# Kernel optimization log

Measured on AMD Instinct MI355X. Metric: run time of the kernel, lower is better.

## Reference

```python
import jax, jax.numpy as jnp
import numpy as np

C = 128   # channels
C4 = C // 4

def setup_inputs() -> dict:
    key = jax.random.key(0)
    k1, k2, k3, k4, k5 = jax.random.split(key, 5)
    B, N = 16, 2048
    x_h = jax.random.normal(k1, (B, C, N), dtype=jnp.float32)
    x_o = jax.random.normal(k2, (B, C, N), dtype=jnp.float32)
    # q_conv and k_conv share the SAME weight (tied in __init__), bias=False
    w_qk = jax.random.normal(k3, (C4, C), dtype=jnp.float32) * (1.0 / np.sqrt(C))
    # v_conv: Conv1d(C, C, 1) with bias
    w_v = jax.random.normal(k4, (C, C), dtype=jnp.float32) * (1.0 / np.sqrt(C))
    b_v = jax.random.normal(k5, (C,), dtype=jnp.float32) * 0.01
    return {"x_h": x_h, "x_o": x_o, "w_qk": w_qk, "w_v": w_v, "b_v": b_v}

def reference(x_h, x_o, w_qk, w_v, b_v):
    # SA_Layer_1 forward (only layer used by Grasp_Transformer_Last.forward)
    # 1x1 conv == channel matmul
    xh_q = jnp.einsum('dc,bcn->bnd', w_qk, x_h)            # [B, Nh, C4]
    xo_k = jnp.einsum('dc,bcm->bdm', w_qk, x_o)            # [B, C4, No]
    alpha = jnp.einsum('bnd,bdm->bnm', xh_q, xo_k)         # [B, Nh, No]
    # no softmax: normalize by column sums over dim=1 (Nh axis)
    attention = alpha / (1e-9 + jnp.sum(alpha, axis=1, keepdims=True))
    xo_v = jnp.einsum('dc,bcm->bmd', w_v, x_o) + b_v       # [B, No, C]
    x_r = jnp.einsum('bnm,bmd->bnd', attention, xo_v)      # [B, Nh, C]
    x_r = jnp.transpose(x_r, (0, 2, 1))                    # [B, C, Nh]
    return (x_r, attention)
```

## Files before the change

### kernel.cpp

```cpp
#include <hip/hip_runtime.h>

constexpr int NTOK = 2048;
constexpr int CH   = 128;
constexpr int C4   = 32;
constexpr int NB   = 16;

typedef __attribute__((ext_vector_type(8))) __bf16 bf16x8;
typedef __attribute__((ext_vector_type(4))) float  f32x4;

__device__ __forceinline__ unsigned short f2bf(float f) {
  union { float f; unsigned u; } v; v.f = f;
  unsigned r = v.u + 0x7fffu + ((v.u >> 16) & 1u);
  return (unsigned short)(r >> 16);
}
__device__ __forceinline__ float bf2f(unsigned short h) {
  union { unsigned u; float f; } v; v.u = ((unsigned)h) << 16;
  return v.f;
}

__global__ __launch_bounds__(256) void rs_kernel(const float* __restrict__ x_h,
                                                 double* __restrict__ rowsumH) {
  const int t = threadIdx.x;
  const int c0 = blockIdx.x * 16;
  const int b = blockIdx.y;
  __shared__ double red[4];
  for (int cl = 0; cl < 16; ++cl) {
    const float* rp = x_h + (size_t)(b * CH + c0 + cl) * NTOK;
    double s = 0.0;
    for (int i = 0; i < 2; ++i) {
      float4 v = *(const float4*)(rp + (t + 256 * i) * 4);
      s += (double)v.x + (double)v.y + (double)v.z + (double)v.w;
    }
    for (int off = 1; off <= 32; off <<= 1) s += __shfl_xor(s, off);
    if ((t & 63) == 0) red[t >> 6] = s;
    __syncthreads();
    if (t == 0) rowsumH[b * CH + c0 + cl] = red[0] + red[1] + red[2] + red[3];
    __syncthreads();
  }
}

__global__ __launch_bounds__(256) void p_kernel(const double* __restrict__ rowsumH,
                                                const float* __restrict__ w_qk,
                                                double* __restrict__ P) {
  const int t = threadIdx.x, b = blockIdx.x;
  __shared__ double Sl[C4];
  if (t < C4) {
    double s = 0.0;
    for (int c = 0; c < CH; ++c) s += (double)w_qk[t * CH + c] * rowsumH[b * CH + c];
    Sl[t] = s;
  }
  __syncthreads();
  if (t < CH) {
    double p = 0.0;
    for (int d = 0; d < C4; ++d) p += Sl[d] * (double)w_qk[d * CH + t];
    P[b * CH + t] = p;
  }
}

__global__ __launch_bounds__(256) void prep_qk(const float* __restrict__ x_h,
                                               const float* __restrict__ x_o,
                                               const float* __restrict__ w_qk,
                                               float* __restrict__ xhq_f32,
                                               float* __restrict__ xokT_f32,
                                               unsigned short* __restrict__ xhq_hi,
                                               unsigned short* __restrict__ xokT_hi,
                                               unsigned short* __restrict__ xhq_lo,
                                               unsigned short* __restrict__ xokT_lo) {
  const int t = threadIdx.x;
  const int n0 = blockIdx.x * 64;
  const int b = blockIdx.y;
  const int which = blockIdx.z;
  const float* src = which ? x_o : x_h;
  float* dstf = which ? xokT_f32 : xhq_f32;
  unsigned short* dsth = which ? xokT_hi : xhq_hi;
  unsigned short* dstl = which ? xokT_lo : xhq_lo;

  __shared__ float Xt[CH][64];
  __shared__ float Wl[C4][132];

  for (int i = 0; i < 8; ++i) {
    int flat = t + 256 * i;
    int c = flat >> 4, f4 = flat & 15;
    float4 v = *(const float4*)(src + (size_t)(b * CH + c) * NTOK + n0 + f4 * 4);
    *(float4*)&Xt[c][f4 * 4] = v;
  }
  for (int i = 0; i < 4; ++i) {
    int flat = t + 256 * i;
    int d = flat >> 5, f4 = flat & 31;
    float4 v = *(const float4*)(w_qk + d * CH + f4 * 4);
    *(float4*)&Wl[d][f4 * 4] = v;
  }
  __syncthreads();

  const int nb = (t & 15) * 4;
  const int d0 = (t >> 4) * 2;
  float acc[4][2] = {};
#pragma unroll 4
  for (int c = 0; c < CH; ++c) {
    float4 x4 = *(const float4*)&Xt[c][nb];
    float w0 = Wl[d0][c], w1 = Wl[d0 + 1][c];
    acc[0][0] += x4.x * w0; acc[0][1] += x4.x * w1;
    acc[1][0] += x4.y * w0; acc[1][1] += x4.y * w1;
    acc[2][0] += x4.z * w0; acc[2][1] += x4.z * w1;
    acc[3][0] += x4.w * w0; acc[3][1] += x4.w * w1;
  }

  const size_t robase = (size_t)(b * NTOK + n0 + nb);
#pragma unroll
  for (int i = 0; i < 4; ++i) {
    size_t base = (robase + i) * C4 + d0;
    *(float2*)(dstf + base) = make_float2(acc[i][0], acc[i][1]);
    unsigned short h0 = f2bf(acc[i][0]), h1 = f2bf(acc[i][1]);
    *(unsigned*)(dsth + base) = (unsigned)h0 | ((unsigned)h1 << 16);
    unsigned short l0 = f2bf(acc[i][0] - bf2f(h0));
    unsigned short l1 = f2bf(acc[i][1] - bf2f(h1));
    *(unsigned*)(dstl + base) = (unsigned)l0 | ((unsigned)l1 << 16);
  }
}

__global__ __launch_bounds__(256) void inv_s2(const float* __restrict__ x_o,
                                              const double* __restrict__ P,
                                              const float* __restrict__ xokT_f32,
                                              float* __restrict__ inv,
                                              float* __restrict__ S2) {
  const int t = threadIdx.x;
  const int b = blockIdx.y;
  const int m = blockIdx.x * 256 + t;
  __shared__ double Pl[CH];
  __shared__ float S2l[C4];
  if (t < CH) Pl[t] = P[b * CH + t];
  if (t < C4) S2l[t] = 0.f;
  __syncthreads();
  double cs = 0.0;
  const float* xp = x_o + (size_t)b * CH * NTOK + m;
#pragma unroll 8
  for (int c = 0; c < CH; ++c) cs += Pl[c] * (double)xp[(size_t)c * NTOK];
  float iv = (float)(1.0 / (1e-9 + cs));
  inv[b * NTOK + m] = iv;
  const float* rp = xokT_f32 + (size_t)(b * NTOK + m) * C4;
  for (int dd = 0; dd < C4; ++dd) {
    int d2 = (dd + t) & 31;
    atomicAdd(&S2l[d2], rp[d2] * iv);
  }
  __syncthreads();
  if (t < C4) atomicAdd(&S2[b * C4 + t], S2l[t]);
}

__global__ __launch_bounds__(256) void u_kernel(const float* __restrict__ x_o,
                                                const float* __restrict__ xokT_f32,
                                                const float* __restrict__ inv,
                                                float* __restrict__ U) {
  const int t = threadIdx.x;
  const int c0 = blockIdx.x * 8;
  const int mbase0 = blockIdx.y * 512;
  const int b = blockIdx.z;
  const int d = t & 31, cl = t >> 5;
  __shared__ float Xs[8][256];
  float acc = 0.f;
  for (int cc = 0; cc < 2; ++cc) {
    const int mb = mbase0 + cc * 256;
    __syncthreads();
    for (int i = 0; i < 2; ++i) {
      int flat = t + 256 * i;
      int row = flat >> 6, f4 = flat & 63;
      float4 xv = *(const float4*)(x_o + (size_t)(b * CH + c0 + row) * NTOK + mb + f4 * 4);
      float4 iv = *(const float4*)(inv + b * NTOK + mb + f4 * 4);
      xv.x *= iv.x; xv.y *= iv.y; xv.z *= iv.z; xv.w *= iv.w;
      *(float4*)&Xs[row][f4 * 4] = xv;
    }
    __syncthreads();
    const float* ap = xokT_f32 + (size_t)(b * NTOK + mb) * C4 + d;
#pragma unroll 4
    for (int mm = 0; mm < 256; mm += 4) {
      float4 xq = *(const float4*)&Xs[cl][mm];
      float a0 = ap[(mm + 0) * C4];
      float a1 = ap[(mm + 1) * C4];
      float a2 = ap[(mm + 2) * C4];
      float a3 = ap[(mm + 3) * C4];
      acc += a0 * xq.x + a1 * xq.y + a2 * xq.z + a3 * xq.w;
    }
  }
  atomicAdd(&U[(size_t)(b * C4 + d) * CH + c0 + cl], acc);
}

__global__ __launch_bounds__(256) void t_kernel(const float* __restrict__ U,
                                                const float* __restrict__ w_v,
                                                const float* __restrict__ b_v,
                                                const float* __restrict__ S2,
                                                float* __restrict__ T) {
  const int t = threadIdx.x, b = blockIdx.x;
  __shared__ float Wl[CH * CH];
  for (int i = 0; i < 16; ++i) {
    int flat = t + 256 * i;
    *(float4*)&Wl[flat * 4] = *(const float4*)(w_v + flat * 4);
  }
  __syncthreads();
  const int d = t & 31;
  const int cg = (t >> 5) * 16;
  float acc[16] = {};
  const float* up = U + (size_t)(b * C4 + d) * CH;
  for (int cp = 0; cp < CH; ++cp) {
    float u = up[cp];
#pragma unroll
    for (int j = 0; j < 16; ++j) acc[j] += u * Wl[(cg + j) * CH + cp];
  }
  float s2 = S2[b * C4 + d];
#pragma unroll
  for (int j = 0; j < 16; ++j) acc[j] += s2 * b_v[cg + j];
  float* tp = T + (size_t)(b * C4 + d) * CH + cg;
#pragma unroll
  for (int j = 0; j < 16; j += 4)
    *(float4*)(tp + j) = make_float4(acc[j], acc[j + 1], acc[j + 2], acc[j + 3]);
}

__global__ __launch_bounds__(256) void xr_kernel(const float* __restrict__ xhq_f32,
                                                 const float* __restrict__ T,
                                                 float* __restrict__ out0) {
  const int t = threadIdx.x;
  const int n = blockIdx.x * 256 + t;
  const int b = blockIdx.y;
  __shared__ float Tl[CH][36];
  for (int i = 0; i < 16; ++i) {
    int flat = t + 256 * i;
    int d = flat >> 7, c = flat & 127;
    Tl[c][d] = T[(size_t)b * C4 * CH + flat];
  }
  __syncthreads();
  float xq[C4];
  const float* qp = xhq_f32 + (size_t)(b * NTOK + n) * C4;
#pragma unroll
  for (int i = 0; i < 8; ++i) {
    float4 v = *(const float4*)(qp + i * 4);
    xq[i * 4] = v.x; xq[i * 4 + 1] = v.y; xq[i * 4 + 2] = v.z; xq[i * 4 + 3] = v.w;
  }
  float* op = out0 + (size_t)b * CH * NTOK + n;
  for (int c = 0; c < CH; ++c) {
    float acc = 0.f;
#pragma unroll
    for (int dd = 0; dd < C4; dd += 4) {
      float4 tv = *(const float4*)&Tl[c][dd];
      acc += xq[dd] * tv.x + xq[dd + 1] * tv.y + xq[dd + 2] * tv.z + xq[dd + 3] * tv.w;
    }
    op[(size_t)c * NTOK] = acc;
  }
}

__global__ __launch_bounds__(256) void attn_kernel(const unsigned short* __restrict__ xhq_hi,
                                                   const unsigned short* __restrict__ xhq_lo,
                                                   const unsigned short* __restrict__ xokT_hi,
                                                   const unsigned short* __restrict__ xokT_lo,
                                                   const float* __restrict__ inv,
                                                   float* __restrict__ out1) {
  const int t = threadIdx.x;
  const int wave = t >> 6, lane = t & 63;
  const int quad = lane >> 4, l16 = lane & 15;
  const int m0 = blockIdx.x * 64;
  const int n0 = blockIdx.y * 64;
  const int b = blockIdx.z;

  const int n = n0 + wave * 16 + l16;
  const size_t abase = (size_t)(b * NTOK + n) * C4 + quad * 8;
  bf16x8 ah = *(const bf16x8*)(const void*)(xhq_hi + abase);
  bf16x8 al = *(const bf16x8*)(const void*)(xhq_lo + abase);

  bf16x8 bh[4], bl[4];
  float invv[4];
#pragma unroll
  for (int tt = 0; tt < 4; ++tt) {
    int m = m0 + tt * 16 + l16;
    size_t bbase = (size_t)(b * NTOK + m) * C4 + quad * 8;
    bh[tt] = *(const bf16x8*)(const void*)(xokT_hi + bbase);
    bl[tt] = *(const bf16x8*)(const void*)(xokT_lo + bbase);
    invv[tt] = inv[b * NTOK + m];
  }

  const int nrow = n0 + wave * 16 + quad * 4;
#pragma unroll
  for (int tt = 0; tt < 4; ++tt) {
    f32x4 z = {0.f, 0.f, 0.f, 0.f};
    f32x4 acc = __builtin_amdgcn_mfma_f32_16x16x32_bf16(al, bh[tt], z, 0, 0, 0);
    acc = __builtin_amdgcn_mfma_f32_16x16x32_bf16(ah, bl[tt], acc, 0, 0, 0);
    acc = __builtin_amdgcn_mfma_f32_16x16x32_bf16(ah, bh[tt], acc, 0, 0, 0);
#pragma unroll
    for (int r = 0; r < 4; ++r) {
      float v = acc[r] * invv[tt];
      size_t off = ((size_t)(b * NTOK) + nrow + r) * NTOK + m0 + tt * 16 + l16;
      __builtin_nontemporal_store(v, out1 + off);
    }
  }
}

extern "C" void kernel_launch(void* const* d_in, const int* in_sizes, int n_in,
                              void* d_out, int out_size, void* d_ws, size_t ws_size,
                              hipStream_t stream) {
  (void)in_sizes; (void)n_in; (void)out_size; (void)ws_size;
  const float* x_h  = (const float*)d_in[0];
  const float* x_o  = (const float*)d_in[1];
  const float* w_qk = (const float*)d_in[2];
  const float* w_v  = (const float*)d_in[3];
  const float* b_v  = (const float*)d_in[4];
  float* out0 = (float*)d_out;
  float* out1 = out0 + (size_t)NB * CH * NTOK;

  char* ws = (char*)d_ws;
  float* xhq_f32        = (float*)(ws + 0);
  float* xokT_f32       = (float*)(ws + 4194304);
  unsigned short* xhq_hi  = (unsigned short*)(ws + 8388608);
  unsigned short* xokT_hi = (unsigned short*)(ws + 10485760);
  unsigned short* xhq_lo  = (unsigned short*)(ws + 12582912);
  unsigned short* xokT_lo = (unsigned short*)(ws + 14680064);
  float* inv      = (float*)(ws + 16777216);
  float* S2       = (float*)(ws + 16908288);
  float* U        = (float*)(ws + 16910336);
  float* T        = (float*)(ws + 17172480);
  double* rowsumH = (double*)(ws + 17434624);
  double* P       = (double*)(ws + 17450880);

  hipMemsetAsync(S2, 0, 2048 + 262144, stream);

  rs_kernel <<<dim3(8, NB), 256, 0, stream>>>(x_h, rowsumH);
  p_kernel  <<<NB, 256, 0, stream>>>(rowsumH, w_qk, P);
  prep_qk   <<<dim3(32, NB, 2), 256, 0, stream>>>(x_h, x_o, w_qk, xhq_f32, xokT_f32,
                                                  xhq_hi, xokT_hi, xhq_lo, xokT_lo);
  inv_s2    <<<dim3(8, NB), 256, 0, stream>>>(x_o, P, xokT_f32, inv, S2);
  u_kernel  <<<dim3(16, 4, NB), 256, 0, stream>>>(x_o, xokT_f32, inv, U);
  t_kernel  <<<NB, 256, 0, stream>>>(U, w_v, b_v, S2, T);
  xr_kernel <<<dim3(8, NB), 256, 0, stream>>>(xhq_f32, T, out0);
  attn_kernel<<<dim3(32, 32, NB), 256, 0, stream>>>(xhq_hi, xhq_lo, xokT_hi, xokT_lo,
                                                    inv, out1);
}
```

Baseline: 447.2 us.

## Fold P and inverse column-sum into prep_qk, drop atomics and memset

```diff
diff --git a/kernel.cpp b/kernel.cpp
--- a/kernel.cpp
+++ b/kernel.cpp
@@ -20,52 +20,31 @@
 
 __global__ __launch_bounds__(256) void rs_kernel(const float* __restrict__ x_h,
                                                  double* __restrict__ rowsumH) {
-  const int t = threadIdx.x;
-  const int c0 = blockIdx.x * 16;
+  const int lane = threadIdx.x & 63;
+  const int c = blockIdx.x * 4 + (threadIdx.x >> 6);
   const int b = blockIdx.y;
-  __shared__ double red[4];
-  for (int cl = 0; cl < 16; ++cl) {
-    const float* rp = x_h + (size_t)(b * CH + c0 + cl) * NTOK;
-    double s = 0.0;
-    for (int i = 0; i < 2; ++i) {
-      float4 v = *(const float4*)(rp + (t + 256 * i) * 4);
-      s += (double)v.x + (double)v.y + (double)v.z + (double)v.w;
-    }
-    for (int off = 1; off <= 32; off <<= 1) s += __shfl_xor(s, off);
-    if ((t & 63) == 0) red[t >> 6] = s;
-    __syncthreads();
-    if (t == 0) rowsumH[b * CH + c0 + cl] = red[0] + red[1] + red[2] + red[3];
-    __syncthreads();
-  }
-}
-
-__global__ __launch_bounds__(256) void p_kernel(const double* __restrict__ rowsumH,
-                                                const float* __restrict__ w_qk,
-                                                double* __restrict__ P) {
-  const int t = threadIdx.x, b = blockIdx.x;
-  __shared__ double Sl[C4];
-  if (t < C4) {
-    double s = 0.0;
-    for (int c = 0; c < CH; ++c) s += (double)w_qk[t * CH + c] * rowsumH[b * CH + c];
-    Sl[t] = s;
-  }
-  __syncthreads();
-  if (t < CH) {
-    double p = 0.0;
-    for (int d = 0; d < C4; ++d) p += Sl[d] * (double)w_qk[d * CH + t];
-    P[b * CH + t] = p;
-  }
+  const float* rp = x_h + (size_t)(b * CH + c) * NTOK;
+  double s = 0.0;
+#pragma unroll
+  for (int i = 0; i < 8; ++i) {
+    float4 v = *(const float4*)(rp + (lane + 64 * i) * 4);
+    s += (double)v.x + (double)v.y + (double)v.z + (double)v.w;
+  }
+  for (int off = 1; off <= 32; off <<= 1) s += __shfl_xor(s, off);
+  if (lane == 0) rowsumH[b * CH + c] = s;
 }
 
 __global__ __launch_bounds__(256) void prep_qk(const float* __restrict__ x_h,
                                                const float* __restrict__ x_o,
                                                const float* __restrict__ w_qk,
+                                               const double* __restrict__ rowsumH,
                                                float* __restrict__ xhq_f32,
                                                float* __restrict__ xokT_f32,
                                                unsigned short* __restrict__ xhq_hi,
                                                unsigned short* __restrict__ xokT_hi,
                                                unsigned short* __restrict__ xhq_lo,
-                                               unsigned short* __restrict__ xokT_lo) {
+                                               unsigned short* __restrict__ xokT_lo,
+                                               float* __restrict__ inv) {
   const int t = threadIdx.x;
   const int n0 = blockIdx.x * 64;
   const int b = blockIdx.y;
@@ -77,6 +56,8 @@
 
   __shared__ float Xt[CH][64];
   __shared__ float Wl[C4][132];
+  __shared__ double Sl[C4];
+  __shared__ double Pl[CH];
 
   for (int i = 0; i < 8; ++i) {
     int flat = t + 256 * i;
@@ -116,43 +97,36 @@
     unsigned short l1 = f2bf(acc[i][1] - bf2f(h1));
     *(unsigned*)(dstl + base) = (unsigned)l0 | ((unsigned)l1 << 16);
   }
-}
-
-__global__ __launch_bounds__(256) void inv_s2(const float* __restrict__ x_o,
-                                              const double* __restrict__ P,
-                                              const float* __restrict__ xokT_f32,
-                                              float* __restrict__ inv,
-                                              float* __restrict__ S2) {
-  const int t = threadIdx.x;
-  const int b = blockIdx.y;
-  const int m = blockIdx.x * 256 + t;
-  __shared__ double Pl[CH];
-  __shared__ float S2l[C4];
-  if (t < CH) Pl[t] = P[b * CH + t];
-  if (t < C4) S2l[t] = 0.f;
-  __syncthreads();
-  double cs = 0.0;
-  const float* xp = x_o + (size_t)b * CH * NTOK + m;
-#pragma unroll 8
-  for (int c = 0; c < CH; ++c) cs += Pl[c] * (double)xp[(size_t)c * NTOK];
-  float iv = (float)(1.0 / (1e-9 + cs));
-  inv[b * NTOK + m] = iv;
-  const float* rp = xokT_f32 + (size_t)(b * NTOK + m) * C4;
-  for (int dd = 0; dd < C4; ++dd) {
-    int d2 = (dd + t) & 31;
-    atomicAdd(&S2l[d2], rp[d2] * iv);
-  }
-  __syncthreads();
-  if (t < C4) atomicAdd(&S2[b * C4 + t], S2l[t]);
+
+  if (which) {
+    if (t < C4) {
+      double s = 0.0;
+      for (int c = 0; c < CH; ++c) s += (double)Wl[t][c] * rowsumH[b * CH + c];
+      Sl[t] = s;
+    }
+    __syncthreads();
+    if (t < CH) {
+      double p = 0.0;
+      for (int d = 0; d < C4; ++d) p += Sl[d] * (double)Wl[d][t];
+      Pl[t] = p;
+    }
+    __syncthreads();
+    if (t < 64) {
+      double s = 0.0;
+      for (int c = 0; c < CH; ++c) s += Pl[c] * (double)Xt[c][t];
+      inv[b * NTOK + n0 + t] = (float)(1.0 / (1e-9 + s));
+    }
+  }
 }
 
 __global__ __launch_bounds__(256) void u_kernel(const float* __restrict__ x_o,
                                                 const float* __restrict__ xokT_f32,
                                                 const float* __restrict__ inv,
-                                                float* __restrict__ U) {
+                                                float* __restrict__ U4) {
   const int t = threadIdx.x;
   const int c0 = blockIdx.x * 8;
-  const int mbase0 = blockIdx.y * 512;
+  const int slab = blockIdx.y;
+  const int mbase0 = slab * 512;
   const int b = blockIdx.z;
   const int d = t & 31, cl = t >> 5;
   __shared__ float Xs[8][256];
@@ -180,31 +154,43 @@
       acc += a0 * xq.x + a1 * xq.y + a2 * xq.z + a3 * xq.w;
     }
   }
-  atomicAdd(&U[(size_t)(b * C4 + d) * CH + c0 + cl], acc);
-}
-
-__global__ __launch_bounds__(256) void t_kernel(const float* __restrict__ U,
+  U4[(size_t)((b * 4 + slab) * C4 + d) * CH + c0 + cl] = acc;
+}
+
+__global__ __launch_bounds__(256) void t_kernel(const float* __restrict__ U4,
                                                 const float* __restrict__ w_v,
                                                 const float* __restrict__ b_v,
-                                                const float* __restrict__ S2,
+                                                const float* __restrict__ xokT_f32,
+                                                const float* __restrict__ inv,
                                                 float* __restrict__ T) {
   const int t = threadIdx.x, b = blockIdx.x;
   __shared__ float Wl[CH * CH];
+  __shared__ float S2s[8][C4];
+  const int d = t & 31;
+  const int g = t >> 5;
+  {
+    const float* kp = xokT_f32 + (size_t)b * NTOK * C4;
+    const float* ip = inv + b * NTOK;
+    float s = 0.f;
+    for (int m = g * 256; m < g * 256 + 256; ++m) s += kp[(size_t)m * C4 + d] * ip[m];
+    S2s[g][d] = s;
+  }
   for (int i = 0; i < 16; ++i) {
     int flat = t + 256 * i;
     *(float4*)&Wl[flat * 4] = *(const float4*)(w_v + flat * 4);
   }
   __syncthreads();
-  const int d = t & 31;
-  const int cg = (t >> 5) * 16;
+  float s2 = 0.f;
+#pragma unroll
+  for (int gg = 0; gg < 8; ++gg) s2 += S2s[gg][d];
+  const int cg = g * 16;
   float acc[16] = {};
-  const float* up = U + (size_t)(b * C4 + d) * CH;
+  const float* up = U4 + (size_t)(b * 4 * C4 + d) * CH;
   for (int cp = 0; cp < CH; ++cp) {
-    float u = up[cp];
+    float u = up[cp] + up[C4 * CH + cp] + up[2 * C4 * CH + cp] + up[3 * C4 * CH + cp];
 #pragma unroll
     for (int j = 0; j < 16; ++j) acc[j] += u * Wl[(cg + j) * CH + cp];
   }
-  float s2 = S2[b * C4 + d];
 #pragma unroll
   for (int j = 0; j < 16; ++j) acc[j] += s2 * b_v[cg + j];
   float* tp = T + (size_t)(b * C4 + d) * CH + cg;
@@ -310,21 +296,16 @@
   unsigned short* xhq_lo  = (unsigned short*)(ws + 12582912);
   unsigned short* xokT_lo = (unsigned short*)(ws + 14680064);
   float* inv      = (float*)(ws + 16777216);
-  float* S2       = (float*)(ws + 16908288);
-  float* U        = (float*)(ws + 16910336);
-  float* T        = (float*)(ws + 17172480);
-  double* rowsumH = (double*)(ws + 17434624);
-  double* P       = (double*)(ws + 17450880);
-
-  hipMemsetAsync(S2, 0, 2048 + 262144, stream);
-
-  rs_kernel <<<dim3(8, NB), 256, 0, stream>>>(x_h, rowsumH);
-  p_kernel  <<<NB, 256, 0, stream>>>(rowsumH, w_qk, P);
-  prep_qk   <<<dim3(32, NB, 2), 256, 0, stream>>>(x_h, x_o, w_qk, xhq_f32, xokT_f32,
-                                                  xhq_hi, xokT_hi, xhq_lo, xokT_lo);
-  inv_s2    <<<dim3(8, NB), 256, 0, stream>>>(x_o, P, xokT_f32, inv, S2);
-  u_kernel  <<<dim3(16, 4, NB), 256, 0, stream>>>(x_o, xokT_f32, inv, U);
-  t_kernel  <<<NB, 256, 0, stream>>>(U, w_v, b_v, S2, T);
+  float* U4       = (float*)(ws + 16908288);
+  float* T        = (float*)(ws + 17956864);
+  double* rowsumH = (double*)(ws + 18219008);
+
+  rs_kernel <<<dim3(32, NB), 256, 0, stream>>>(x_h, rowsumH);
+  prep_qk   <<<dim3(32, NB, 2), 256, 0, stream>>>(x_h, x_o, w_qk, rowsumH,
+                                                  xhq_f32, xokT_f32,
+                                                  xhq_hi, xokT_hi, xhq_lo, xokT_lo, inv);
+  u_kernel  <<<dim3(16, 4, NB), 256, 0, stream>>>(x_o, xokT_f32, inv, U4);
+  t_kernel  <<<NB, 256, 0, stream>>>(U4, w_v, b_v, xokT_f32, inv, T);
   xr_kernel <<<dim3(8, NB), 256, 0, stream>>>(xhq_f32, T, out0);
   attn_kernel<<<dim3(32, 32, NB), 256, 0, stream>>>(xhq_hi, xhq_lo, xokT_hi, xokT_lo,
                                                     inv, out1);
```

New measurement: 427.1 us. -4.5%, faster.
